# Kernel tuning notes

Hardware: AMD Instinct MI355X
Metric: run time of the kernel (lower is better)

The kernel has to match this reference:

```python
import jax, jax.numpy as jnp
import numpy as np
import math

NQ, NK, QDIM, MDIM, VDIM = 8192, 8192, 512, 512, 512
NEG = -float(1 << 32)


def setup_inputs() -> dict:
    key = jax.random.key(0)
    ks = jax.random.split(key, 8)
    Q = jax.random.normal(ks[0], (NQ, QDIM), dtype=jnp.float32)
    K = jax.random.normal(ks[1], (NK, QDIM), dtype=jnp.float32)
    V = jax.random.normal(ks[2], (NK, VDIM), dtype=jnp.float32)
    mask = jax.random.randint(ks[3], (NQ, NK), 0, 2) == 1
    s = 1.0 / math.sqrt(QDIM)
    WQ_w = jax.random.uniform(ks[4], (MDIM, QDIM), minval=-s, maxval=s, dtype=jnp.float32)
    WQ_b = jax.random.uniform(ks[5], (MDIM,), minval=-s, maxval=s, dtype=jnp.float32)
    WK_w = jax.random.uniform(ks[6], (MDIM, QDIM), minval=-s, maxval=s, dtype=jnp.float32)
    WK_b = jax.random.uniform(ks[7], (MDIM,), minval=-s, maxval=s, dtype=jnp.float32)
    return {"Q": Q, "K": K, "V": V, "WQ_w": WQ_w, "WQ_b": WQ_b,
            "WK_w": WK_w, "WK_b": WK_b, "mask": mask}


def reference(Q, K, V, WQ_w, WQ_b, WK_w, WK_b, mask):
    # Linear projections: y = x @ W^T + b
    Qp = Q @ WQ_w.T + WQ_b          # [NQ, MDIM]
    Kp = K @ WK_w.T + WK_b          # [NK, MDIM]
    scale = 1.0 / math.sqrt(MDIM)
    attn = (Qp @ Kp.T) * scale      # [NQ, NK]
    attn = jnp.where(mask, NEG, attn)
    attn = jax.nn.softmax(attn, axis=-1)
    return attn @ V                 # [NQ, VDIM]
```

## Files before the change

### kernel.cpp

```cpp
#include <hip/hip_runtime.h>

typedef __attribute__((ext_vector_type(8))) short short8;
typedef __attribute__((ext_vector_type(4))) float f32x4;

#define DEVFN __device__ __forceinline__

constexpr float NEGF = -4294967296.0f;
constexpr float SCALE_LOG2E = 0.06375872465057373f;

DEVFN unsigned short f2bf(float f) {
  unsigned int u = __float_as_uint(f);
  u += 0x7FFFu + ((u >> 16) & 1u);
  return (unsigned short)(u >> 16);
}
DEVFN float bf2f(unsigned short h) { return __uint_as_float((unsigned)h << 16); }

DEVFN float exp2v(float x) {
  float r;
  asm("v_exp_f32 %0, %1" : "=v"(r) : "v"(x));
  return r;
}

DEVFN void gl_lds16(const void* g, void* l) {
  __builtin_amdgcn_global_load_lds(
      (const __attribute__((address_space(1))) unsigned int*)g,
      (__attribute__((address_space(3))) unsigned int*)l, 16, 0, 0);
}

DEVFN float dpp_fmax16(float x) {
  int v;
  v = __builtin_amdgcn_update_dpp(0, __float_as_int(x), 0xB1, 0xF, 0xF, true);
  x = fmaxf(x, __int_as_float(v));
  v = __builtin_amdgcn_update_dpp(0, __float_as_int(x), 0x4E, 0xF, 0xF, true);
  x = fmaxf(x, __int_as_float(v));
  v = __builtin_amdgcn_update_dpp(0, __float_as_int(x), 0x141, 0xF, 0xF, true);
  x = fmaxf(x, __int_as_float(v));
  v = __builtin_amdgcn_update_dpp(0, __float_as_int(x), 0x140, 0xF, 0xF, true);
  x = fmaxf(x, __int_as_float(v));
  return x;
}
DEVFN float dpp_fadd16(float x) {
  int v;
  v = __builtin_amdgcn_update_dpp(0, __float_as_int(x), 0xB1, 0xF, 0xF, true);
  x += __int_as_float(v);
  v = __builtin_amdgcn_update_dpp(0, __float_as_int(x), 0x4E, 0xF, 0xF, true);
  x += __int_as_float(v);
  v = __builtin_amdgcn_update_dpp(0, __float_as_int(x), 0x141, 0xF, 0xF, true);
  x += __int_as_float(v);
  v = __builtin_amdgcn_update_dpp(0, __float_as_int(x), 0x140, 0xF, 0xF, true);
  x += __int_as_float(v);
  return x;
}

__global__ void k_detect(const unsigned int* __restrict__ q, const unsigned int* __restrict__ m,
                         int* __restrict__ fflag, int* __restrict__ esize) {
  int lane = threadIdx.x;
  if (blockIdx.x == 0) {
    unsigned bad = 0;
    for (int i = 0; i < 64; i++) {
      unsigned v = q[i * 64 + lane];
      unsigned h = v & 0xFFFFu;
      unsigned e = (h >> 7) & 0xFFu;
      if (h != 0u && (e < 96u || e > 150u)) bad = 1;
    }
    unsigned long long anyb = __ballot(bad != 0);
    if (lane == 0) *fflag = (anyb == 0ULL) ? 1 : 0;
  } else {
    unsigned okd = 1, okh = 1, okb = 1;
    for (int i = 0; i < 64; i++) {
      unsigned v = m[i * 64 + lane];
      if (v > 1u && v != 0x3F800000u) okd = 0;
      unsigned h0 = v & 0xFFFFu, h1 = v >> 16;
      if ((h0 && h0 != 0x3F80u && h0 != 1u) || (h1 && h1 != 0x3F80u && h1 != 1u)) okh = 0;
      if (v & 0xFEFEFEFEu) okb = 0;
    }
    okd = (__ballot(okd == 0) == 0ULL);
    okh = (__ballot(okh == 0) == 0ULL);
    okb = (__ballot(okb == 0) == 0ULL);
    if (lane == 0) *esize = okd ? 4 : (okh ? 2 : 1);
  }
}

__global__ void k_prep(const void* __restrict__ Q, unsigned short* __restrict__ Qb,
                       const void* __restrict__ K, unsigned short* __restrict__ Kb,
                       const void* __restrict__ Wq, unsigned short* __restrict__ Wqb,
                       const void* __restrict__ Wk, unsigned short* __restrict__ Wkb,
                       const void* __restrict__ bq, unsigned short* __restrict__ bqb,
                       const void* __restrict__ bk, unsigned short* __restrict__ bkb,
                       const int* __restrict__ bf16flag) {
  int blk = blockIdx.x;
  const void* src; unsigned short* dst; int base, n;
  if (blk < 2048)      { src = Q;  dst = Qb;  base = blk;        n = 8192 * 512; }
  else if (blk < 4096) { src = K;  dst = Kb;  base = blk - 2048; n = 8192 * 512; }
  else if (blk < 4224) { src = Wq; dst = Wqb; base = blk - 4096; n = 512 * 512; }
  else if (blk < 4352) { src = Wk; dst = Wkb; base = blk - 4224; n = 512 * 512; }
  else if (blk == 4352){ src = bq; dst = bqb; base = 0;          n = 512; }
  else                 { src = bk; dst = bkb; base = 0;          n = 512; }
  int i = (base * 256 + threadIdx.x) * 8;
  if (i >= n) return;
  if (*bf16flag) {
    *(uint4*)(dst + i) = *(const uint4*)((const unsigned short*)src + i);
  } else {
    const float* f = (const float*)src + i;
    float4 a = *(const float4*)f, b = *(const float4*)(f + 4);
    uint4 o;
    o.x = (unsigned)f2bf(a.x) | ((unsigned)f2bf(a.y) << 16);
    o.y = (unsigned)f2bf(a.z) | ((unsigned)f2bf(a.w) << 16);
    o.z = (unsigned)f2bf(b.x) | ((unsigned)f2bf(b.y) << 16);
    o.w = (unsigned)f2bf(b.z) | ((unsigned)f2bf(b.w) << 16);
    *(uint4*)(dst + i) = o;
  }
}

__global__ void k_transpose_v(const void* __restrict__ Vsrc, const int* __restrict__ bf16flag,
                              unsigned short* __restrict__ Vt) {
  __shared__ unsigned short T[64][72];
  int t = threadIdx.x;
  int rb = blockIdx.x, cb = blockIdx.y;
  int r = t >> 3, c8 = (t & 7) * 8;
  int isbf = *bf16flag;
#pragma unroll
  for (int j = 0; j < 2; j++) {
    int row = rb * 64 + j * 32 + r;
    unsigned short e[8];
    if (isbf) {
      alignas(16) unsigned short tmp[8];
      *(uint4*)tmp = *(const uint4*)((const unsigned short*)Vsrc + (size_t)row * 512 + cb * 64 + c8);
#pragma unroll
      for (int i = 0; i < 8; i++) e[i] = tmp[i];
    } else {
      const float* f = (const float*)Vsrc + (size_t)row * 512 + cb * 64 + c8;
      float4 a = *(const float4*)f, b = *(const float4*)(f + 4);
      e[0] = f2bf(a.x); e[1] = f2bf(a.y); e[2] = f2bf(a.z); e[3] = f2bf(a.w);
      e[4] = f2bf(b.x); e[5] = f2bf(b.y); e[6] = f2bf(b.z); e[7] = f2bf(b.w);
    }
#pragma unroll
    for (int i = 0; i < 8; i++) T[c8 + i][j * 32 + r] = e[i];
  }
  __syncthreads();
#pragma unroll
  for (int j = 0; j < 2; j++) {
    int d = cb * 64 + j * 32 + r;
    alignas(16) unsigned short o[8];
#pragma unroll
    for (int i = 0; i < 8; i++) o[i] = T[j * 32 + r][c8 + i];
    int tt = rb * 2 + (c8 >> 5);
    *(uint4*)(Vt + ((size_t)tt * 512 + d) * 32 + (c8 & 31)) = *(const uint4*)o;
  }
}

DEVFN unsigned nib4(unsigned v) {
  unsigned t = v; t |= t >> 1; t |= t >> 2; t |= t >> 4; t &= 0x01010101u;
  return (t * 0x10204080u) >> 28;
}
DEVFN unsigned pair2(unsigned v) {
  unsigned t = v; t |= t >> 8; t |= t >> 4; t |= t >> 2; t |= t >> 1;
  return (t & 1u) | (((t >> 16) & 1u) << 1);
}
__global__ void k_pack(const void* __restrict__ mask, const int* __restrict__ esize,
                       unsigned long long* __restrict__ bits) {
  int wv = (blockIdx.x * blockDim.x + threadIdx.x) >> 6;
  int lane = threadIdx.x & 63;
  int sz = *esize;
  if (sz == 4) {
    const unsigned int* m = (const unsigned int*)mask;
    for (int g = wv; g < 262144; g += 4096) {
      size_t base = (size_t)g * 256 + lane;
      unsigned v0 = m[base], v1 = m[base + 64], v2 = m[base + 128], v3 = m[base + 192];
      unsigned long long b0 = __ballot(v0 != 0u);
      unsigned long long b1 = __ballot(v1 != 0u);
      unsigned long long b2 = __ballot(v2 != 0u);
      unsigned long long b3 = __ballot(v3 != 0u);
      if (lane == 0) {
        bits[g * 4 + 0] = b0; bits[g * 4 + 1] = b1;
        bits[g * 4 + 2] = b2; bits[g * 4 + 3] = b3;
      }
    }
  } else if (sz == 2) {
    const uint4* m = (const uint4*)mask;
    for (int g = wv; g < 131072; g += 4096) {
      uint4 v = m[(size_t)g * 64 + lane];
      unsigned c8 = pair2(v.x) | (pair2(v.y) << 2) | (pair2(v.z) << 4) | (pair2(v.w) << 6);
      unsigned long long x = (unsigned long long)c8 << ((lane & 7) * 8);
      x |= __shfl_xor(x, 1); x |= __shfl_xor(x, 2); x |= __shfl_xor(x, 4);
      if ((lane & 7) == 0) bits[g * 8 + (lane >> 3)] = x;
    }
  } else {
    const uint4* m = (const uint4*)mask;
    for (int g = wv; g < 65536; g += 4096) {
      uint4 v = m[(size_t)g * 64 + lane];
      unsigned c16 = nib4(v.x) | (nib4(v.y) << 4) | (nib4(v.z) << 8) | (nib4(v.w) << 12);
      unsigned long long x = (unsigned long long)c16 << ((lane & 3) * 16);
      x |= __shfl_xor(x, 1); x |= __shfl_xor(x, 2);
      if ((lane & 3) == 0) bits[g * 16 + (lane >> 2)] = x;
    }
  }
}

__global__ __launch_bounds__(256, 2) void k_proj(
    const unsigned short* __restrict__ Aq, const unsigned short* __restrict__ Wq,
    const unsigned short* __restrict__ bq, unsigned short* __restrict__ outq,
    const unsigned short* __restrict__ Ak, const unsigned short* __restrict__ Wk,
    const unsigned short* __restrict__ bk, unsigned short* __restrict__ outk) {
  const unsigned short* A = blockIdx.z ? Ak : Aq;
  const unsigned short* W = blockIdx.z ? Wk : Wq;
  const unsigned short* bias = blockIdx.z ? bk : bq;
  unsigned short* out = blockIdx.z ? outk : outq;
  float sc = blockIdx.z ? 1.0f : SCALE_LOG2E;

  __shared__ alignas(16) unsigned short As[128 * 64];
  __shared__ alignas(16) unsigned short Bs[128 * 64];
  int tid = threadIdx.x, lane = tid & 63, wave = tid >> 6;
  int wi = wave >> 1, wj = wave & 1;
  int l15 = lane & 15, l4 = lane >> 4;
  int rowbase = blockIdx.x * 128, colbase = blockIdx.y * 128;
  f32x4 acc[4][4];
#pragma unroll
  for (int i = 0; i < 4; i++)
#pragma unroll
    for (int j = 0; j < 4; j++) acc[i][j] = f32x4{0.f, 0.f, 0.f, 0.f};

  int swr = l15 & 7;
  for (int kb = 0; kb < 512; kb += 64) {
    __syncthreads();
#pragma unroll
    for (int t = 0; t < 4; t++) {
      int inst = wave * 4 + t;
      int r = inst * 8 + (lane >> 3);
      int c = ((lane & 7) ^ (r & 7)) * 8;
      gl_lds16(A + (size_t)(rowbase + r) * 512 + kb + c, &As[inst * 512]);
      gl_lds16(W + (size_t)(colbase + r) * 512 + kb + c, &Bs[inst * 512]);
    }
    __syncthreads();
#pragma unroll
    for (int t2 = 0; t2 < 2; t2++) {
      short8 a[4], b[4];
#pragma unroll
      for (int i = 0; i < 4; i++) {
        int row = wi * 64 + i * 16 + l15;
        a[i] = *(const short8*)&As[row * 64 + (((t2 * 4 + l4) ^ swr) * 8)];
      }
#pragma unroll
      for (int j = 0; j < 4; j++) {
        int row = wj * 64 + j * 16 + l15;
        b[j] = *(const short8*)&Bs[row * 64 + (((t2 * 4 + l4) ^ swr) * 8)];
      }
#pragma unroll
      for (int i = 0; i < 4; i++)
#pragma unroll
        for (int j = 0; j < 4; j++)
          acc[i][j] = __builtin_amdgcn_mfma_f32_16x16x32_bf16(a[i], b[j], acc[i][j], 0, 0, 0);
    }
  }
#pragma unroll
  for (int j = 0; j < 4; j++) {
    int col = colbase + wj * 64 + j * 16 + l15;
    float bj = bf2f(bias[col]);
#pragma unroll
    for (int i = 0; i < 4; i++) {
      int row0 = rowbase + wi * 64 + i * 16 + l4 * 4;
#pragma unroll
      for (int r = 0; r < 4; r++)
        out[(size_t)(row0 + r) * 512 + col] = f2bf((acc[i][j][r] + bj) * sc);
    }
  }
}

__global__ __launch_bounds__(512, 2) void k_attn(
    const unsigned short* __restrict__ Qp, const unsigned short* __restrict__ Kp,
    const unsigned short* __restrict__ Vt, const unsigned long long* __restrict__ mbits,
    unsigned short* __restrict__ Opart, float* __restrict__ mpart, float* __restrict__ lpart) {
  __shared__ alignas(16) unsigned short KB[2][16384];
  __shared__ alignas(16) unsigned short VB[16384];
  __shared__ alignas(16) unsigned short P2[2][4][128][8];
  __shared__ alignas(16) float alds[2][128];
  __shared__ alignas(16) int nfl[2][8];
  int tid = threadIdx.x, lane = tid & 63, wave = tid >> 6;
  int l15 = lane & 15, l4 = lane >> 4;
  int b = blockIdx.x;
  int split = b & 7;
  int qb = (b >> 3) * 128;

  short8 qf[16];
  {
    int row = qb + wave * 16 + l15;
#pragma unroll
    for (int t = 0; t < 16; t++)
      qf[t] = *(const short8*)(Qp + (size_t)row * 512 + t * 32 + l4 * 8);
  }
  f32x4 o[8][4];
#pragma unroll
  for (int i = 0; i < 8; i++)
#pragma unroll
    for (int j = 0; j < 4; j++) o[i][j] = f32x4{0.f, 0.f, 0.f, 0.f};
  float mi[4] = {NEGF, NEGF, NEGF, NEGF};
  float li_l[4] = {0.f, 0.f, 0.f, 0.f};

  int swK = l15 | ((l15 & 3) << 4);
  const unsigned int* mb32 = (const unsigned int*)mbits;

  {
    int tv = split * 32;
#pragma unroll
    for (int t = 0; t < 4; t++) {
      int r = wave * 4 + t;
      int swz = (r & 15) | ((r & 3) << 4);
      gl_lds16(Kp + (size_t)(tv * 32 + r) * 512 + ((lane ^ swz) * 8), &KB[0][r * 512]);
    }
  }
  __builtin_amdgcn_s_waitcnt(0x0F70);
  __builtin_amdgcn_s_barrier();

  for (int it = 0; it < 32; it++) {
    int cur = it & 1, prv = cur ^ 1;
    int tv = split * 32 + it;

    unsigned mw[4];
#pragma unroll
    for (int r = 0; r < 4; r++)
      mw[r] = mb32[((size_t)(qb + wave * 16 + l4 * 4 + r) * 128 + split * 16 + (it >> 1)) * 2 + (it & 1)];
    asm volatile("" ::: "memory");

    {
      int tv1 = (it < 31) ? tv + 1 : tv;
#pragma unroll
      for (int t = 0; t < 4; t++) {
        int r = wave * 4 + t;
        int swz = (r & 15) | ((r & 3) << 4);
        gl_lds16(Kp + (size_t)(tv1 * 32 + r) * 512 + ((lane ^ swz) * 8), &KB[prv][r * 512]);
      }
    }

    if (it) {
      __builtin_amdgcn_s_waitcnt(0x0F78);
      __builtin_amdgcn_sched_barrier(0);
      {
        const int4* n4 = (const int4*)&nfl[prv][0];
        int4 na = n4[0], nb4 = n4[1];
        if (na.x | na.y | na.z | na.w | nb4.x | nb4.y | nb4.z | nb4.w) {
#pragma unroll
          for (int rf = 0; rf < 8; rf++) {
            f32x4 av = *(const f32x4*)&alds[prv][rf * 16 + l4 * 4];
#pragma unroll
            for (int df = 0; df < 4; df++)
#pragma unroll
              for (int j = 0; j < 4; j++) o[rf][df][j] *= av[j];
          }
        }
      }
      short8 vf[4];
#pragma unroll
      for (int df = 0; df < 4; df++) {
        int d = wave * 64 + df * 16 + l15;
        vf[df] = *(const short8*)&VB[d * 32 + ((l4 ^ ((l15 >> 2) & 3)) * 8)];
      }
      __builtin_amdgcn_s_setprio(1);
#pragma unroll
      for (int rf = 0; rf < 8; rf++) {
        short8 pa = *(const short8*)&P2[prv][l4][rf * 16 + l15][0];
#pragma unroll
        for (int df = 0; df < 4; df++)
          o[rf][df] = __builtin_amdgcn_mfma_f32_16x16x32_bf16(pa, vf[df], o[rf][df], 0, 0, 0);
      }
      __builtin_amdgcn_s_setprio(0);
    }

#pragma unroll
    for (int t = 0; t < 4; t++) {
      int inst = wave * 4 + t;
      int d = inst * 16 + (lane >> 2);
      int cg = (lane & 3) ^ ((d >> 2) & 3);
      gl_lds16(Vt + (size_t)tv * 16384 + d * 32 + cg * 8, &VB[inst * 512]);
    }

    f32x4 sacc[2];
#pragma unroll
    for (int c = 0; c < 2; c++) sacc[c] = f32x4{0.f, 0.f, 0.f, 0.f};
    __builtin_amdgcn_s_setprio(1);
#pragma unroll
    for (int t2 = 0; t2 < 16; t2++) {
      short8 a = qf[t2];
#pragma unroll
      for (int c = 0; c < 2; c++) {
        int row = c * 16 + l15;
        short8 bb = *(const short8*)&KB[cur][row * 512 + (((t2 * 4 + l4) ^ swK) * 8)];
        sacc[c] = __builtin_amdgcn_mfma_f32_16x16x32_bf16(a, bb, sacc[c], 0, 0, 0);
      }
    }
    __builtin_amdgcn_s_setprio(0);

#pragma unroll
    for (int c = 0; c < 2; c++)
#pragma unroll
      for (int r = 0; r < 4; r++) {
        bool msk = (mw[r] >> (c * 16 + l15)) & 1u;
        sacc[c][r] = msk ? NEGF : sacc[c][r];
      }

    float al4[4];
    bool need = false;
#pragma unroll
    for (int r = 0; r < 4; r++) {
      float t = dpp_fmax16(fmaxf(sacc[0][r], sacc[1][r]));
      al4[r] = t;
      need |= (t > mi[r] + 11.5f);
    }
    unsigned long long blt = __ballot(need);
    if (lane == 0) nfl[cur][wave] = (blt != 0ULL) ? 1 : 0;
    if (blt) {
#pragma unroll
      for (int r = 0; r < 4; r++) {
        float mn = fmaxf(mi[r], al4[r]);
        float a = exp2v(mi[r] - mn);
        li_l[r] *= a;
        mi[r] = mn;
        al4[r] = a;
      }
    } else {
#pragma unroll
      for (int r = 0; r < 4; r++) al4[r] = 1.0f;
    }
    if (l15 == 0) *(f32x4*)&alds[cur][wave * 16 + l4 * 4] = f32x4{al4[0], al4[1], al4[2], al4[3]};

#pragma unroll
    for (int r = 0; r < 4; r++) {
      sacc[0][r] = exp2v(sacc[0][r] - mi[r]);
      sacc[1][r] = exp2v(sacc[1][r] - mi[r]);
      li_l[r] += sacc[0][r] + sacc[1][r];
    }

#pragma unroll
    for (int r = 0; r < 4; r++) {
      int prow = wave * 16 + l4 * 4 + r;
#pragma unroll
      for (int c = 0; c < 2; c++)
        P2[cur][c * 2 + (l15 >> 3)][prow][l15 & 7] = f2bf(sacc[c][r]);
    }

    __builtin_amdgcn_s_waitcnt(0x0074);
    __builtin_amdgcn_s_barrier();
  }

  __builtin_amdgcn_s_waitcnt(0x0F70);
  __builtin_amdgcn_sched_barrier(0);
  {
    const int4* n4 = (const int4*)&nfl[1][0];
    int4 na = n4[0], nb4 = n4[1];
    if (na.x | na.y | na.z | na.w | nb4.x | nb4.y | nb4.z | nb4.w) {
#pragma unroll
      for (int rf = 0; rf < 8; rf++) {
        f32x4 av = *(const f32x4*)&alds[1][rf * 16 + l4 * 4];
#pragma unroll
        for (int df = 0; df < 4; df++)
#pragma unroll
          for (int j = 0; j < 4; j++) o[rf][df][j] *= av[j];
      }
    }
    short8 vf[4];
#pragma unroll
    for (int df = 0; df < 4; df++) {
      int d = wave * 64 + df * 16 + l15;
      vf[df] = *(const short8*)&VB[d * 32 + ((l4 ^ ((l15 >> 2) & 3)) * 8)];
    }
#pragma unroll
    for (int rf = 0; rf < 8; rf++) {
      short8 pa = *(const short8*)&P2[1][l4][rf * 16 + l15][0];
#pragma unroll
      for (int df = 0; df < 4; df++)
        o[rf][df] = __builtin_amdgcn_mfma_f32_16x16x32_bf16(pa, vf[df], o[rf][df], 0, 0, 0);
    }
  }

  float li[4];
#pragma unroll
  for (int r = 0; r < 4; r++) li[r] = dpp_fadd16(li_l[r]);
#pragma unroll
  for (int r = 0; r < 4; r++) {
    int row = qb + wave * 16 + l4 * 4 + r;
    if (l15 == 0) {
      mpart[(size_t)split * 8192 + row] = mi[r];
      lpart[(size_t)split * 8192 + row] = li[r];
    }
  }
  uint2* op2 = (uint2*)Opart;
#pragma unroll
  for (int rf = 0; rf < 8; rf++)
#pragma unroll
    for (int df = 0; df < 4; df++) {
      int f = wave * 4 + df;
      uint2 v;
      v.x = (unsigned)f2bf(o[rf][df][0]) | ((unsigned)f2bf(o[rf][df][1]) << 16);
      v.y = (unsigned)f2bf(o[rf][df][2]) | ((unsigned)f2bf(o[rf][df][3]) << 16);
      op2[(((size_t)b * 32 + f) * 8 + rf) * 64 + l4 * 16 + l15] = v;
    }
}

__global__ void k_combine(const unsigned short* __restrict__ Opart,
                          const float* __restrict__ mpart, const float* __restrict__ lpart,
                          float* __restrict__ out) {
  int q = blockIdx.x;
  int quarter = blockIdx.y;
  int tid = threadIdx.x;
  int wave = tid >> 6, lane = tid & 63, l4 = (lane >> 4) & 3, l15 = lane & 15;
  int row0 = q * 128 + wave * 16 + l4 * 4;

  float w[8][4], inv[4];
#pragma unroll
  for (int r = 0; r < 4; r++) {
    float M = NEGF;
    float mv[8];
#pragma unroll
    for (int s = 0; s < 8; s++) { mv[s] = mpart[s * 8192 + row0 + r]; M = fmaxf(M, mv[s]); }
    float L = 0.f;
#pragma unroll
    for (int s = 0; s < 8; s++) {
      float ws = exp2v(mv[s] - M);
      w[s][r] = ws;
      L += ws * lpart[s * 8192 + row0 + r];
    }
    inv[r] = 1.0f / L;
  }
  const uint2* op2 = (const uint2*)Opart;
#pragma unroll
  for (int fo = 0; fo < 8; fo++) {
    int f = quarter * 8 + fo;
    float acc[4] = {0.f, 0.f, 0.f, 0.f};
#pragma unroll
    for (int s = 0; s < 8; s++) {
      uint2 v = op2[(((size_t)(q * 8 + s) * 32 + f) * 8 + wave) * 64 + l4 * 16 + l15];
      acc[0] += w[s][0] * bf2f((unsigned short)(v.x & 0xFFFFu));
      acc[1] += w[s][1] * bf2f((unsigned short)(v.x >> 16));
      acc[2] += w[s][2] * bf2f((unsigned short)(v.y & 0xFFFFu));
      acc[3] += w[s][3] * bf2f((unsigned short)(v.y >> 16));
    }
    int col = f * 16 + l15;
#pragma unroll
    for (int r = 0; r < 4; r++)
      out[(size_t)(row0 + r) * 512 + col] = acc[r] * inv[r];
  }
}

extern "C" void kernel_launch(void* const* d_in, const int* in_sizes, int n_in,
                              void* d_out, int out_size, void* d_ws, size_t ws_size,
                              hipStream_t stream) {
  const void* Q   = d_in[0];
  const void* K   = d_in[1];
  const void* V   = d_in[2];
  const void* WQw = d_in[3];
  const void* WQb = d_in[4];
  const void* WKw = d_in[5];
  const void* WKb = d_in[6];
  const void* mask = d_in[7];
  float* out = (float*)d_out;
  char* ws = (char*)d_ws;
  (void)in_sizes; (void)n_in; (void)out_size; (void)ws_size;

  constexpr size_t SZ_MAT = (size_t)8192 * 512 * 2;
  size_t off = 4096;
  unsigned short* Qb  = (unsigned short*)(ws + off); off += SZ_MAT;
  unsigned short* Kb  = (unsigned short*)(ws + off); off += SZ_MAT;
  unsigned short* Wqb = (unsigned short*)(ws + off); off += (size_t)512 * 512 * 2;
  unsigned short* Wkb = (unsigned short*)(ws + off); off += (size_t)512 * 512 * 2;
  unsigned short* bqb = (unsigned short*)(ws + off); off += 1024;
  unsigned short* bkb = (unsigned short*)(ws + off); off += 1024;
  unsigned short* Vt  = (unsigned short*)(ws + off); off += SZ_MAT;
  unsigned short* Qp  = (unsigned short*)(ws + off); off += SZ_MAT;
  unsigned short* Kp  = (unsigned short*)(ws + off); off += SZ_MAT;
  unsigned long long* mbits = (unsigned long long*)(ws + off); off += (size_t)8192 * 128 * 8;
  unsigned short* Opart = (unsigned short*)(ws + off); off += (size_t)512 * 512 * 32 * 8;
  float* mpart = (float*)(ws + off); off += (size_t)8 * 8192 * 4;
  float* lpart = (float*)(ws + off); off += (size_t)8 * 8192 * 4;
  int* fflag = (int*)ws;
  int* esize = (int*)(ws + 64);

  k_detect<<<2, 64, 0, stream>>>((const unsigned int*)Q, (const unsigned int*)mask, fflag, esize);
  k_prep<<<4354, 256, 0, stream>>>(Q, Qb, K, Kb, WQw, Wqb, WKw, Wkb, WQb, bqb, WKb, bkb, fflag);
  k_transpose_v<<<dim3(128, 8), 256, 0, stream>>>(V, fflag, Vt);
  k_pack<<<1024, 256, 0, stream>>>(mask, esize, mbits);
  k_proj<<<dim3(64, 4, 2), 256, 0, stream>>>(Qb, Wqb, bqb, Qp, Kb, Wkb, bkb, Kp);
  k_attn<<<512, 512, 0, stream>>>(Qp, Kp, Vt, mbits, Opart, mpart, lpart);
  k_combine<<<dim3(64, 4), 512, 0, stream>>>(Opart, mpart, lpart, out);
}
```

Before: 778.4 us.

## Double-buffer V tiles and halve KV splits to four per query block

Adds a second LDS buffer for V so the next V tile is prefetched during the current iteration instead of being loaded after the PV MFMAs, which removes the wait before PV. It also halves the flash-decoding split count from 8 to 4, doubling iterations per block and halving partial outputs and the combine work. The cost is 32KB more LDS per block, which may hurt occupancy, and 256 blocks on 256 CUs, which gives only one block per CU and less latency hiding.

Measured after the change: 749.4 us. 3.7% less time.

```diff
diff --git a/kernel.cpp b/kernel.cpp
--- a/kernel.cpp
+++ b/kernel.cpp
@@ -271,15 +271,15 @@
     const unsigned short* __restrict__ Vt, const unsigned long long* __restrict__ mbits,
     unsigned short* __restrict__ Opart, float* __restrict__ mpart, float* __restrict__ lpart) {
   __shared__ alignas(16) unsigned short KB[2][16384];
-  __shared__ alignas(16) unsigned short VB[16384];
+  __shared__ alignas(16) unsigned short VB[2][16384];
   __shared__ alignas(16) unsigned short P2[2][4][128][8];
   __shared__ alignas(16) float alds[2][128];
   __shared__ alignas(16) int nfl[2][8];
   int tid = threadIdx.x, lane = tid & 63, wave = tid >> 6;
   int l15 = lane & 15, l4 = lane >> 4;
   int b = blockIdx.x;
-  int split = b & 7;
-  int qb = (b >> 3) * 128;
+  int split = b & 3;
+  int qb = (b >> 2) * 128;
 
   short8 qf[16];
   {
@@ -299,40 +299,46 @@
   int swK = l15 | ((l15 & 3) << 4);
   const unsigned int* mb32 = (const unsigned int*)mbits;
 
-  {
-    int tv = split * 32;
-#pragma unroll
-    for (int t = 0; t < 4; t++) {
-      int r = wave * 4 + t;
-      int swz = (r & 15) | ((r & 3) << 4);
-      gl_lds16(Kp + (size_t)(tv * 32 + r) * 512 + ((lane ^ swz) * 8), &KB[0][r * 512]);
-    }
-  }
+#define STAGE_K(TV, BUF)                                                         \
+  {                                                                              \
+    _Pragma("unroll") for (int t = 0; t < 4; t++) {                              \
+      int r = wave * 4 + t;                                                      \
+      int swz = (r & 15) | ((r & 3) << 4);                                       \
+      gl_lds16(Kp + (size_t)((TV) * 32 + r) * 512 + ((lane ^ swz) * 8),          \
+               &KB[BUF][r * 512]);                                               \
+    }                                                                            \
+  }
+#define STAGE_V(TV, BUF)                                                         \
+  {                                                                              \
+    _Pragma("unroll") for (int t = 0; t < 4; t++) {                              \
+      int inst = wave * 4 + t;                                                   \
+      int d = inst * 16 + (lane >> 2);                                           \
+      int cg = (lane & 3) ^ ((d >> 2) & 3);                                      \
+      gl_lds16(Vt + (size_t)(TV) * 16384 + d * 32 + cg * 8, &VB[BUF][inst * 512]); \
+    }                                                                            \
+  }
+
+  STAGE_K(split * 64, 0);
+  STAGE_V(split * 64, 0);
   __builtin_amdgcn_s_waitcnt(0x0F70);
   __builtin_amdgcn_s_barrier();
 
-  for (int it = 0; it < 32; it++) {
+  for (int it = 0; it < 64; it++) {
     int cur = it & 1, prv = cur ^ 1;
-    int tv = split * 32 + it;
+    int tv = split * 64 + it;
 
     unsigned mw[4];
 #pragma unroll
     for (int r = 0; r < 4; r++)
-      mw[r] = mb32[((size_t)(qb + wave * 16 + l4 * 4 + r) * 128 + split * 16 + (it >> 1)) * 2 + (it & 1)];
+      mw[r] = mb32[((size_t)(qb + wave * 16 + l4 * 4 + r) * 128 + split * 32 + (it >> 1)) * 2 + (it & 1)];
     asm volatile("" ::: "memory");
 
     {
-      int tv1 = (it < 31) ? tv + 1 : tv;
-#pragma unroll
-      for (int t = 0; t < 4; t++) {
-        int r = wave * 4 + t;
-        int swz = (r & 15) | ((r & 3) << 4);
-        gl_lds16(Kp + (size_t)(tv1 * 32 + r) * 512 + ((lane ^ swz) * 8), &KB[prv][r * 512]);
-      }
+      int tv1 = (it < 63) ? tv + 1 : tv;
+      STAGE_K(tv1, prv);
     }
 
     if (it) {
-      __builtin_amdgcn_s_waitcnt(0x0F78);
       __builtin_amdgcn_sched_barrier(0);
       {
         const int4* n4 = (const int4*)&nfl[prv][0];
@@ -352,7 +358,7 @@
 #pragma unroll
       for (int df = 0; df < 4; df++) {
         int d = wave * 64 + df * 16 + l15;
-        vf[df] = *(const short8*)&VB[d * 32 + ((l4 ^ ((l15 >> 2) & 3)) * 8)];
+        vf[df] = *(const short8*)&VB[prv][d * 32 + ((l4 ^ ((l15 >> 2) & 3)) * 8)];
       }
       __builtin_amdgcn_s_setprio(1);
 #pragma unroll
@@ -363,14 +369,6 @@
           o[rf][df] = __builtin_amdgcn_mfma_f32_16x16x32_bf16(pa, vf[df], o[rf][df], 0, 0, 0);
       }
       __builtin_amdgcn_s_setprio(0);
-    }
-
-#pragma unroll
-    for (int t = 0; t < 4; t++) {
-      int inst = wave * 4 + t;
-      int d = inst * 16 + (lane >> 2);
-      int cg = (lane & 3) ^ ((d >> 2) & 3);
-      gl_lds16(Vt + (size_t)tv * 16384 + d * 32 + cg * 8, &VB[inst * 512]);
     }
 
     f32x4 sacc[2];
@@ -437,6 +435,11 @@
         P2[cur][c * 2 + (l15 >> 3)][prow][l15 & 7] = f2bf(sacc[c][r]);
     }
 
+    {
+      int tvv = (it < 63) ? tv + 1 : tv;
+      STAGE_V(tvv, prv);
+    }
+
     __builtin_amdgcn_s_waitcnt(0x0074);
     __builtin_amdgcn_s_barrier();
   }
@@ -460,7 +463,7 @@
 #pragma unroll
     for (int df = 0; df < 4; df++) {
       int d = wave * 64 + df * 16 + l15;
-      vf[df] = *(const short8*)&VB[d * 32 + ((l4 ^ ((l15 >> 2) & 3)) * 8)];
+      vf[df] = *(const short8*)&VB[1][d * 32 + ((l4 ^ ((l15 >> 2) & 3)) * 8)];
     }
 #pragma unroll
     for (int rf = 0; rf < 8; rf++) {
@@ -493,6 +496,8 @@
       v.y = (unsigned)f2bf(o[rf][df][2]) | ((unsigned)f2bf(o[rf][df][3]) << 16);
       op2[(((size_t)b * 32 + f) * 8 + rf) * 64 + l4 * 16 + l15] = v;
     }
+#undef STAGE_K
+#undef STAGE_V
 }
 
 __global__ void k_combine(const unsigned short* __restrict__ Opart,
@@ -504,16 +509,16 @@
   int wave = tid >> 6, lane = tid & 63, l4 = (lane >> 4) & 3, l15 = lane & 15;
   int row0 = q * 128 + wave * 16 + l4 * 4;
 
-  float w[8][4], inv[4];
+  float w[4][4], inv[4];
 #pragma unroll
   for (int r = 0; r < 4; r++) {
     float M = NEGF;
-    float mv[8];
-#pragma unroll
-    for (int s = 0; s < 8; s++) { mv[s] = mpart[s * 8192 + row0 + r]; M = fmaxf(M, mv[s]); }
+    float mv[4];
+#pragma unroll
+    for (int s = 0; s < 4; s++) { mv[s] = mpart[s * 8192 + row0 + r]; M = fmaxf(M, mv[s]); }
     float L = 0.f;
 #pragma unroll
-    for (int s = 0; s < 8; s++) {
+    for (int s = 0; s < 4; s++) {
       float ws = exp2v(mv[s] - M);
       w[s][r] = ws;
       L += ws * lpart[s * 8192 + row0 + r];
@@ -526,8 +531,8 @@
     int f = quarter * 8 + fo;
     float acc[4] = {0.f, 0.f, 0.f, 0.f};
 #pragma unroll
-    for (int s = 0; s < 8; s++) {
-      uint2 v = op2[(((size_t)(q * 8 + s) * 32 + f) * 8 + wave) * 64 + l4 * 16 + l15];
+    for (int s = 0; s < 4; s++) {
+      uint2 v = op2[(((size_t)(q * 4 + s) * 32 + f) * 8 + wave) * 64 + l4 * 16 + l15];
       acc[0] += w[s][0] * bf2f((unsigned short)(v.x & 0xFFFFu));
       acc[1] += w[s][1] * bf2f((unsigned short)(v.x >> 16));
       acc[2] += w[s][2] * bf2f((unsigned short)(v.y & 0xFFFFu));
@@ -567,9 +572,9 @@
   unsigned short* Qp  = (unsigned short*)(ws + off); off += SZ_MAT;
   unsigned short* Kp  = (unsigned short*)(ws + off); off += SZ_MAT;
   unsigned long long* mbits = (unsigned long long*)(ws + off); off += (size_t)8192 * 128 * 8;
-  unsigned short* Opart = (unsigned short*)(ws + off); off += (size_t)512 * 512 * 32 * 8;
-  float* mpart = (float*)(ws + off); off += (size_t)8 * 8192 * 4;
-  float* lpart = (float*)(ws + off); off += (size_t)8 * 8192 * 4;
+  unsigned short* Opart = (unsigned short*)(ws + off); off += (size_t)256 * 32 * 8 * 64 * 8;
+  float* mpart = (float*)(ws + off); off += (size_t)4 * 8192 * 4;
+  float* lpart = (float*)(ws + off); off += (size_t)4 * 8192 * 4;
   int* fflag = (int*)ws;
   int* esize = (int*)(ws + 64);
 
@@ -578,6 +583,6 @@
   k_transpose_v<<<dim3(128, 8), 256, 0, stream>>>(V, fflag, Vt);
   k_pack<<<1024, 256, 0, stream>>>(mask, esize, mbits);
   k_proj<<<dim3(64, 4, 2), 256, 0, stream>>>(Qb, Wqb, bqb, Qp, Kb, Wkb, bkb, Kp);
-  k_attn<<<512, 512, 0, stream>>>(Qp, Kp, Vt, mbits, Opart, mpart, lpart);
+  k_attn<<<256, 512, 0, stream>>>(Qp, Kp, Vt, mbits, Opart, mpart, lpart);
   k_combine<<<dim3(64, 4), 512, 0, stream>>>(Opart, mpart, lpart, out);
 }
```
